# Kernel optimization log

Hardware: AMD Instinct MI355X
Metric: run time of the kernel (lower is better)

Reference implementation:

```python
import jax, jax.numpy as jnp
import numpy as np

N_SYN = 30_000_000
N_POST = 200_000
N_SOURCE = 17_400


def setup_inputs() -> dict:
    key = jax.random.key(0)
    k1, k2, k3, k4 = jax.random.split(key, 4)
    # spike input: ~half of source neurons active (values in {0,1})
    inputs_t = jax.random.randint(k1, (1, N_SOURCE), 0, 2, dtype=jnp.int32)
    # synapse table: col0 = postsynaptic neuron id, col1 = presynaptic source id
    post = jax.random.randint(k2, (N_SYN, 1), 0, N_POST, dtype=jnp.int32)
    pre = jax.random.randint(k3, (N_SYN, 1), 0, N_SOURCE, dtype=jnp.int32)
    indices = jnp.concatenate([post, pre], axis=1)  # [N_SYN, 2]
    weights = jax.random.normal(k4, (N_SYN,), dtype=jnp.float32)
    return {"inputs_t": inputs_t, "indices": indices, "weights": weights, "n_post": N_POST}


def reference(inputs_t, indices, weights, n_post):
    # Original TF code: find active presynaptic columns (inputs_t > 0), gather all
    # synapses whose presynaptic neuron is active (ragged lookup + argsort), then
    # unsorted_segment_sum their weights by postsynaptic id. Mathematically this is:
    #   i_in[post] = sum_{syn : inputs_t[pre[syn]] > 0} weights[syn]
    # which we express as a masked gather + segment_sum (same math, jit-safe).
    active = (inputs_t[0] > 0)                      # [n_source] bool
    pre = indices[:, 1]                             # [n_syn]
    post = indices[:, 0]                            # [n_syn]
    contrib = weights * active[pre].astype(weights.dtype)  # [n_syn]
    i_in = jax.ops.segment_sum(contrib, post, num_segments=n_post)  # [n_post]
    return i_in[None, :]                            # [1, n_post]
```

## Files before the change

kernel.cpp:

```cpp
#include <hip/hip_runtime.h>


typedef int   vint4   __attribute__((ext_vector_type(4)));
typedef float vfloat4 __attribute__((ext_vector_type(4)));
typedef unsigned int uint;

#define P1_BLK    256
#define P1_ITER   12
#define CHUNK     (P1_BLK * P1_ITER * 4)
#define MINICAP   30
#define NB_MAX    392
#define STRIDE_MAX 11744
#define NW_MAX    544
#define P2_BLK    1024
#define NBLK_MAX  2448

__global__ __launch_bounds__(256) void p0_bitmask(
    const int* __restrict__ act, uint* __restrict__ bits_g, int n_src)
{
    int w  = blockIdx.x * blockDim.x + threadIdx.x;
    int nw = (n_src + 31) >> 5;
    if (w < nw) {
        uint m = 0;
        int base = w << 5;
        #pragma unroll
        for (int j = 0; j < 32; ++j) {
            int s = base + j;
            if (s < n_src && act[s] > 0) m |= (1u << j);
        }
        bits_g[w] = m;
    }
}

__global__ __launch_bounds__(P1_BLK) void p1_bucketize(
    const uint* __restrict__ bits_g,
    const vint4* __restrict__ idx4,
    const vfloat4* __restrict__ w4,
    uint* __restrict__ cnt_g,
    uint* __restrict__ pairs_g,
    float* __restrict__ out,
    int sec_base_vec, int sec_nvec, int blocks_s, int nb, int nwords, int stride_dw)
{
    __shared__ uint bits[NW_MAX];
    __shared__ uint cnt[NB_MAX];
    __shared__ __align__(16) uint ord[STRIDE_MAX];

    const int tid = threadIdx.x;
    for (int i = tid; i < nwords; i += P1_BLK) bits[i] = bits_g[i];
    for (int i = tid; i < nb;     i += P1_BLK) cnt[i] = 0;
    __syncthreads();

    const int vbase = sec_base_vec + blockIdx.x * (P1_ITER * P1_BLK);

    for (int it = 0; it < P1_ITER; ++it) {
        int v = vbase + it * P1_BLK + tid;
        if ((v - sec_base_vec) < sec_nvec) {
            vint4   ia = __builtin_nontemporal_load(&idx4[2 * v]);
            vint4   ib = __builtin_nontemporal_load(&idx4[2 * v + 1]);
            vfloat4 wv = __builtin_nontemporal_load(&w4[v]);

            const int   posts[4] = {ia.x, ia.z, ib.x, ib.z};
            const int   pres[4]  = {ia.y, ia.w, ib.y, ib.w};
            const float wsv[4]   = {wv.x, wv.y, wv.z, wv.w};

            #pragma unroll
            for (int j = 0; j < 4; ++j) {
                uint pre = (uint)pres[j];
                if ((bits[pre >> 5] >> (pre & 31u)) & 1u) {
                    uint post = (uint)posts[j];
                    uint b    = post >> 9;
                    uint r    = atomicAdd(&cnt[b], 1u);
                    if (r < MINICAP) {
                        uint pk = (__float_as_uint(wsv[j]) & 0xFFFFFE00u) | (post & 511u);
                        ord[b * MINICAP + r] = pk;
                    } else {
                        atomicAdd(&out[post], wsv[j]);
                    }
                }
            }
        }
    }
    __syncthreads();

    for (int b = tid; b < nb; b += P1_BLK) {
        uint c = cnt[b];
        cnt_g[(size_t)b * (size_t)blocks_s + blockIdx.x] = (c > MINICAP) ? MINICAP : c;
    }
    vint4* dst = (vint4*)(pairs_g + (size_t)blockIdx.x * (size_t)stride_dw);
    const vint4* src = (const vint4*)ord;
    for (int i = tid; i < (stride_dw >> 2); i += P1_BLK)
        dst[i] = src[i];
}

__global__ __launch_bounds__(P2_BLK) void p2_accum(
    const uint* __restrict__ pairs_g,
    const uint* __restrict__ cnt_g,
    float* __restrict__ out,
    int blocks_s, int nb, int stride_dw, int n_post)
{
    __shared__ float hist[512];
    __shared__ unsigned short cntl[NBLK_MAX];

    const int b   = blockIdx.x;
    const int tid = threadIdx.x;
    for (int i = tid; i < 512; i += P2_BLK) hist[i] = 0.f;
    for (int i = tid; i < blocks_s; i += P2_BLK)
        cntl[i] = (unsigned short)cnt_g[(size_t)b * (size_t)blocks_s + i];
    __syncthreads();

    const int total = blocks_s * MINICAP;
    const size_t bucket_off = (size_t)b * MINICAP;
    for (int i = tid; i < total; i += P2_BLK) {
        int blk  = i / MINICAP;
        int slot = i - blk * MINICAP;
        if (slot < (int)cntl[blk]) {
            uint pk = pairs_g[(size_t)blk * (size_t)stride_dw + bucket_off + slot];
            atomicAdd(&hist[pk & 511u], __uint_as_float(pk & 0xFFFFFE00u));
        }
    }
    __syncthreads();

    for (int l = tid; l < 512; l += P2_BLK) {
        int g = (b << 9) + l;
        if (g < n_post) out[g] += hist[l];
    }
}

__global__ __launch_bounds__(256) void syn_scatter_direct(
    const int* __restrict__ act, const vint4* __restrict__ idx4,
    const vfloat4* __restrict__ w4, float* __restrict__ out, int n_vec)
{
    int t = blockIdx.x * blockDim.x + threadIdx.x;
    if (t >= n_vec) return;
    vint4 ia = idx4[2 * t], ib = idx4[2 * t + 1];
    vfloat4 wv = w4[t];
    if (act[ia.y] > 0) atomicAdd(&out[ia.x], wv.x);
    if (act[ia.w] > 0) atomicAdd(&out[ia.z], wv.y);
    if (act[ib.y] > 0) atomicAdd(&out[ib.x], wv.z);
    if (act[ib.w] > 0) atomicAdd(&out[ib.z], wv.w);
}

extern "C" void kernel_launch(void* const* d_in, const int* in_sizes, int n_in,
                              void* d_out, int out_size, void* d_ws, size_t ws_size,
                              hipStream_t stream) {
    const int*   act     = (const int*)d_in[0];
    const int*   indices = (const int*)d_in[1];
    const float* weights = (const float*)d_in[2];

    const int n_src  = in_sizes[0];
    const int n_syn  = in_sizes[2];
    const int n_post = out_size;
    const int n_vec  = n_syn / 4;

    const int nb        = (n_post + 511) >> 9;
    const int nwords    = (n_src + 31) >> 5;
    const int stride_dw = (nb * MINICAP + 31) & ~31;
    const int nblk_tot  = (n_syn + CHUNK - 1) / CHUNK;

    const size_t per_blk_bytes = (size_t)nb * 4 + (size_t)stride_dw * 4;
    const size_t head_bytes    = 4096;
    long long nblk_fit = (ws_size > head_bytes)
                       ? (long long)((ws_size - head_bytes) / per_blk_bytes) : 0;

    bool ok = (n_syn % 4 == 0) && (nb <= NB_MAX - 1) && (nwords <= NW_MAX) &&
              (stride_dw <= STRIDE_MAX) && (nblk_tot <= NBLK_MAX) && (nblk_fit >= 1);
    int nsec = ok ? (int)((nblk_tot + nblk_fit - 1) / nblk_fit) : 1000;

    if (!ok || nsec > 8) {
        (void)hipMemsetAsync(d_out, 0, (size_t)n_post * sizeof(float), stream);
        const int grid = (n_vec + 255) / 256;
        syn_scatter_direct<<<grid, 256, 0, stream>>>(
            act, (const vint4*)indices, (const vfloat4*)weights, (float*)d_out, n_vec);
        return;
    }

    const int nblk_s = (nblk_tot + nsec - 1) / nsec;
    uint* bits_g = (uint*)d_ws;
    uint* cnt_g  = (uint*)((char*)d_ws + head_bytes);
    size_t cnt_bytes = ((size_t)nb * (size_t)nblk_s * 4 + 255) & ~(size_t)255;
    uint* pairs_g = (uint*)((char*)cnt_g + cnt_bytes);

    (void)hipMemsetAsync(d_out, 0, (size_t)n_post * sizeof(float), stream);
    p0_bitmask<<<(nwords + 255) / 256, 256, 0, stream>>>(act, bits_g, n_src);

    const int vec_per_sec = nblk_s * (CHUNK / 4);
    for (int s = 0; s < nsec; ++s) {
        int v0 = s * vec_per_sec;
        int nv = n_vec - v0; if (nv > vec_per_sec) nv = vec_per_sec;
        if (nv <= 0) break;
        int blocks_s = (nv * 4 + CHUNK - 1) / CHUNK;
        p1_bucketize<<<blocks_s, P1_BLK, 0, stream>>>(
            bits_g, (const vint4*)indices, (const vfloat4*)weights,
            cnt_g, pairs_g, (float*)d_out,
            v0, nv, blocks_s, nb, nwords, stride_dw);
        p2_accum<<<nb, P2_BLK, 0, stream>>>(
            pairs_g, cnt_g, (float*)d_out, blocks_s, nb, stride_dw, n_post);
    }
}
```

Baseline: 517.0 us.

## Split bucket accumulation across blocks, pack counters, and software-pipeline bucketize loads

The bucket accumulation pass is split into SPLIT partial histograms per bucket, written to workspace and summed by a new merge kernel, so many more blocks work in parallel than one per bucket. The bucketize kernel shrinks its per-bucket capacity to 16 slots, packs two 16-bit counters per shared word to cut LDS use, sets an occupancy hint, and prefetches the next iteration's loads for full blocks. The accumulation pass now reads the packed pairs as 16-byte vectors. In exchange there are extra kernel launches, partial-sum traffic, and more overflow atomics to global memory because each bucket holds fewer slots.

```diff
diff --git a/kernel.cpp b/kernel.cpp
--- a/kernel.cpp
+++ b/kernel.cpp
@@ -6,14 +6,17 @@
 typedef unsigned int uint;
 
 #define P1_BLK    256
-#define P1_ITER   12
+#define P1_ITER   8
 #define CHUNK     (P1_BLK * P1_ITER * 4)
-#define MINICAP   30
+#define MINICAP   16
 #define NB_MAX    392
-#define STRIDE_MAX 11744
+#define CNTW      ((NB_MAX + 1) / 2)
+#define STRIDE_MAX 6272
 #define NW_MAX    544
-#define P2_BLK    1024
-#define NBLK_MAX  2448
+#define P2_BLK    512
+#define SPLIT     8
+#define NBLK_MAX  3664
+#define CBMAX     ((NBLK_MAX + SPLIT - 1) / SPLIT)
 
 __global__ __launch_bounds__(256) void p0_bitmask(
     const int* __restrict__ act, uint* __restrict__ bits_g, int n_src)
@@ -32,7 +35,7 @@
     }
 }
 
-__global__ __launch_bounds__(P1_BLK) void p1_bucketize(
+__global__ __launch_bounds__(P1_BLK, 5) void p1_bucketize(
     const uint* __restrict__ bits_g,
     const vint4* __restrict__ idx4,
     const vfloat4* __restrict__ w4,
@@ -42,48 +45,68 @@
     int sec_base_vec, int sec_nvec, int blocks_s, int nb, int nwords, int stride_dw)
 {
     __shared__ uint bits[NW_MAX];
-    __shared__ uint cnt[NB_MAX];
+    __shared__ uint cntp[CNTW];
     __shared__ __align__(16) uint ord[STRIDE_MAX];
 
     const int tid = threadIdx.x;
     for (int i = tid; i < nwords; i += P1_BLK) bits[i] = bits_g[i];
-    for (int i = tid; i < nb;     i += P1_BLK) cnt[i] = 0;
+    for (int i = tid; i < CNTW;   i += P1_BLK) cntp[i] = 0;
     __syncthreads();
 
     const int vbase = sec_base_vec + blockIdx.x * (P1_ITER * P1_BLK);
-
-    for (int it = 0; it < P1_ITER; ++it) {
-        int v = vbase + it * P1_BLK + tid;
-        if ((v - sec_base_vec) < sec_nvec) {
-            vint4   ia = __builtin_nontemporal_load(&idx4[2 * v]);
-            vint4   ib = __builtin_nontemporal_load(&idx4[2 * v + 1]);
-            vfloat4 wv = __builtin_nontemporal_load(&w4[v]);
-
-            const int   posts[4] = {ia.x, ia.z, ib.x, ib.z};
-            const int   pres[4]  = {ia.y, ia.w, ib.y, ib.w};
-            const float wsv[4]   = {wv.x, wv.y, wv.z, wv.w};
-
-            #pragma unroll
-            for (int j = 0; j < 4; ++j) {
-                uint pre = (uint)pres[j];
-                if ((bits[pre >> 5] >> (pre & 31u)) & 1u) {
-                    uint post = (uint)posts[j];
-                    uint b    = post >> 9;
-                    uint r    = atomicAdd(&cnt[b], 1u);
-                    if (r < MINICAP) {
-                        uint pk = (__float_as_uint(wsv[j]) & 0xFFFFFE00u) | (post & 511u);
-                        ord[b * MINICAP + r] = pk;
-                    } else {
-                        atomicAdd(&out[post], wsv[j]);
-                    }
+    const bool full = (vbase - sec_base_vec + P1_ITER * P1_BLK) <= sec_nvec;
+
+    auto process = [&](vint4 pa, vint4 pb, vfloat4 pw) {
+        const int   posts[4] = {pa.x, pa.z, pb.x, pb.z};
+        const int   pres[4]  = {pa.y, pa.w, pb.y, pb.w};
+        const float wsv[4]   = {pw.x, pw.y, pw.z, pw.w};
+        #pragma unroll
+        for (int j = 0; j < 4; ++j) {
+            uint pre = (uint)pres[j];
+            if ((bits[pre >> 5] >> (pre & 31u)) & 1u) {
+                uint post = (uint)posts[j];
+                uint b    = post >> 9;
+                uint sh   = (b & 1u) << 4;
+                uint r    = (atomicAdd(&cntp[b >> 1], 1u << sh) >> sh) & 0xFFFFu;
+                if (r < MINICAP) {
+                    uint pk = (__float_as_uint(wsv[j]) & 0xFFFFFE00u) | (post & 511u);
+                    ord[(b << 4) + r] = pk;
+                } else {
+                    atomicAdd(&out[post], wsv[j]);
                 }
             }
         }
+    };
+
+    if (full) {
+        int v = vbase + tid;
+        vint4   ia = __builtin_nontemporal_load(&idx4[2 * v]);
+        vint4   ib = __builtin_nontemporal_load(&idx4[2 * v + 1]);
+        vfloat4 wv = __builtin_nontemporal_load(&w4[v]);
+        for (int it = 0; it < P1_ITER - 1; ++it) {
+            int vn = v + P1_BLK;
+            vint4   na = __builtin_nontemporal_load(&idx4[2 * vn]);
+            vint4   nbv = __builtin_nontemporal_load(&idx4[2 * vn + 1]);
+            vfloat4 nw = __builtin_nontemporal_load(&w4[vn]);
+            process(ia, ib, wv);
+            ia = na; ib = nbv; wv = nw; v = vn;
+        }
+        process(ia, ib, wv);
+    } else {
+        for (int it = 0; it < P1_ITER; ++it) {
+            int v = vbase + it * P1_BLK + tid;
+            if ((v - sec_base_vec) < sec_nvec) {
+                vint4   ia = __builtin_nontemporal_load(&idx4[2 * v]);
+                vint4   ib = __builtin_nontemporal_load(&idx4[2 * v + 1]);
+                vfloat4 wv = __builtin_nontemporal_load(&w4[v]);
+                process(ia, ib, wv);
+            }
+        }
     }
     __syncthreads();
 
     for (int b = tid; b < nb; b += P1_BLK) {
-        uint c = cnt[b];
+        uint c = (cntp[b >> 1] >> ((b & 1u) << 4)) & 0xFFFFu;
         cnt_g[(size_t)b * (size_t)blocks_s + blockIdx.x] = (c > MINICAP) ? MINICAP : c;
     }
     vint4* dst = (vint4*)(pairs_g + (size_t)blockIdx.x * (size_t)stride_dw);
@@ -95,34 +118,60 @@
 __global__ __launch_bounds__(P2_BLK) void p2_accum(
     const uint* __restrict__ pairs_g,
     const uint* __restrict__ cnt_g,
-    float* __restrict__ out,
-    int blocks_s, int nb, int stride_dw, int n_post)
+    float* __restrict__ part,
+    int blocks_s, int nb, int stride_dw)
 {
     __shared__ float hist[512];
-    __shared__ unsigned short cntl[NBLK_MAX];
+    __shared__ unsigned short cntl[CBMAX];
 
     const int b   = blockIdx.x;
+    const int s   = blockIdx.y;
     const int tid = threadIdx.x;
-    for (int i = tid; i < 512; i += P2_BLK) hist[i] = 0.f;
-    for (int i = tid; i < blocks_s; i += P2_BLK)
-        cntl[i] = (unsigned short)cnt_g[(size_t)b * (size_t)blocks_s + i];
-    __syncthreads();
-
-    const int total = blocks_s * MINICAP;
-    const size_t bucket_off = (size_t)b * MINICAP;
+
+    const int chunk = (blocks_s + SPLIT - 1) / SPLIT;
+    const int blk0  = s * chunk;
+    int blkn = blocks_s - blk0;
+    if (blkn > chunk) blkn = chunk;
+    if (blkn < 0) blkn = 0;
+
+    for (int i = tid; i < 512;  i += P2_BLK) hist[i] = 0.f;
+    for (int i = tid; i < blkn; i += P2_BLK)
+        cntl[i] = (unsigned short)cnt_g[(size_t)b * (size_t)blocks_s + blk0 + i];
+    __syncthreads();
+
+    const int total = blkn << 2;
+    const uint boff = ((uint)b) << 4;
     for (int i = tid; i < total; i += P2_BLK) {
-        int blk  = i / MINICAP;
-        int slot = i - blk * MINICAP;
-        if (slot < (int)cntl[blk]) {
-            uint pk = pairs_g[(size_t)blk * (size_t)stride_dw + bucket_off + slot];
-            atomicAdd(&hist[pk & 511u], __uint_as_float(pk & 0xFFFFFE00u));
-        }
-    }
-    __syncthreads();
-
-    for (int l = tid; l < 512; l += P2_BLK) {
-        int g = (b << 9) + l;
-        if (g < n_post) out[g] += hist[l];
+        int bl = i >> 2;
+        int q  = i & 3;
+        const vint4* pv = (const vint4*)(pairs_g
+            + (size_t)(blk0 + bl) * (size_t)stride_dw + boff + (uint)(q << 2));
+        vint4 pk4 = *pv;
+        int c  = (int)cntl[bl];
+        int s0 = q << 2;
+        const uint pks[4] = {(uint)pk4.x, (uint)pk4.y, (uint)pk4.z, (uint)pk4.w};
+        #pragma unroll
+        for (int k = 0; k < 4; ++k) {
+            if (s0 + k < c)
+                atomicAdd(&hist[pks[k] & 511u], __uint_as_float(pks[k] & 0xFFFFFE00u));
+        }
+    }
+    __syncthreads();
+
+    float* dst = part + (size_t)s * ((size_t)nb << 9) + ((size_t)b << 9);
+    for (int l = tid; l < 512; l += P2_BLK) dst[l] = hist[l];
+}
+
+__global__ __launch_bounds__(256) void p3_merge(
+    const float* __restrict__ part, float* __restrict__ out, int n_post, int nb)
+{
+    int g = blockIdx.x * 256 + threadIdx.x;
+    if (g < n_post) {
+        size_t span = (size_t)nb << 9;
+        float acc = 0.f;
+        #pragma unroll
+        for (int k = 0; k < SPLIT; ++k) acc += part[(size_t)k * span + g];
+        out[g] += acc;
     }
 }
 
@@ -157,8 +206,9 @@
     const int stride_dw = (nb * MINICAP + 31) & ~31;
     const int nblk_tot  = (n_syn + CHUNK - 1) / CHUNK;
 
+    const size_t parts_bytes   = ((size_t)SPLIT * ((size_t)nb << 9) * 4 + 255) & ~(size_t)255;
+    const size_t head_bytes    = 4096 + parts_bytes;
     const size_t per_blk_bytes = (size_t)nb * 4 + (size_t)stride_dw * 4;
-    const size_t head_bytes    = 4096;
     long long nblk_fit = (ws_size > head_bytes)
                        ? (long long)((ws_size - head_bytes) / per_blk_bytes) : 0;
 
@@ -175,10 +225,11 @@
     }
 
     const int nblk_s = (nblk_tot + nsec - 1) / nsec;
-    uint* bits_g = (uint*)d_ws;
-    uint* cnt_g  = (uint*)((char*)d_ws + head_bytes);
+    uint*  bits_g = (uint*)d_ws;
+    float* parts  = (float*)((char*)d_ws + 4096);
+    uint*  cnt_g  = (uint*)((char*)d_ws + head_bytes);
     size_t cnt_bytes = ((size_t)nb * (size_t)nblk_s * 4 + 255) & ~(size_t)255;
-    uint* pairs_g = (uint*)((char*)cnt_g + cnt_bytes);
+    uint*  pairs_g = (uint*)((char*)cnt_g + cnt_bytes);
 
     (void)hipMemsetAsync(d_out, 0, (size_t)n_post * sizeof(float), stream);
     p0_bitmask<<<(nwords + 255) / 256, 256, 0, stream>>>(act, bits_g, n_src);
@@ -193,7 +244,9 @@
             bits_g, (const vint4*)indices, (const vfloat4*)weights,
             cnt_g, pairs_g, (float*)d_out,
             v0, nv, blocks_s, nb, nwords, stride_dw);
-        p2_accum<<<nb, P2_BLK, 0, stream>>>(
-            pairs_g, cnt_g, (float*)d_out, blocks_s, nb, stride_dw, n_post);
-    }
-}
+        p2_accum<<<dim3(nb, SPLIT), P2_BLK, 0, stream>>>(
+            pairs_g, cnt_g, parts, blocks_s, nb, stride_dw);
+        p3_merge<<<(n_post + 255) / 256, 256, 0, stream>>>(
+            parts, (float*)d_out, n_post, nb);
+    }
+}
```

Result: faster. 487.0 us (-5.8%).

## Replace bucketize/accumulate pipeline with per-XCC replicated output arrays

Applied to the files above, without the earlier changes.

Drops the two-phase LDS bucketing scheme (per-block bucket slots plus a second accumulation kernel). Instead, each block scatters atomics straight into one of 16 replicated output arrays, picked by the XCC id read from a hardware register and by block parity. A final merge kernel sums the replicas. This keeps atomic traffic local to each XCC's L2 and avoids contention and the pairs buffer round trip, at the cost of a 12.8MB memset and a merge pass.

```diff
diff --git a/kernel.cpp b/kernel.cpp
--- a/kernel.cpp
+++ b/kernel.cpp
@@ -5,15 +5,12 @@
 typedef float vfloat4 __attribute__((ext_vector_type(4)));
 typedef unsigned int uint;
 
-#define P1_BLK    256
-#define P1_ITER   12
-#define CHUNK     (P1_BLK * P1_ITER * 4)
-#define MINICAP   30
-#define NB_MAX    392
-#define STRIDE_MAX 11744
-#define NW_MAX    544
-#define P2_BLK    1024
-#define NBLK_MAX  2448
+#define NW_MAX 544
+#define REP    16
+#define P1_BLK 256
+#define P1_GRID_CAP 2048
+
+#define GETREG_XCC_ID (20 | (0 << 6) | (31 << 11))
 
 __global__ __launch_bounds__(256) void p0_bitmask(
     const int* __restrict__ act, uint* __restrict__ bits_g, int n_src)
@@ -32,97 +29,51 @@
     }
 }
 
-__global__ __launch_bounds__(P1_BLK) void p1_bucketize(
+__global__ __launch_bounds__(P1_BLK) void p1_scatter_rep(
     const uint* __restrict__ bits_g,
     const vint4* __restrict__ idx4,
     const vfloat4* __restrict__ w4,
-    uint* __restrict__ cnt_g,
-    uint* __restrict__ pairs_g,
-    float* __restrict__ out,
-    int sec_base_vec, int sec_nvec, int blocks_s, int nb, int nwords, int stride_dw)
+    float* __restrict__ rep,
+    int n_vec, int n_post, int nwords)
 {
     __shared__ uint bits[NW_MAX];
-    __shared__ uint cnt[NB_MAX];
-    __shared__ __align__(16) uint ord[STRIDE_MAX];
-
     const int tid = threadIdx.x;
     for (int i = tid; i < nwords; i += P1_BLK) bits[i] = bits_g[i];
-    for (int i = tid; i < nb;     i += P1_BLK) cnt[i] = 0;
     __syncthreads();
 
-    const int vbase = sec_base_vec + blockIdx.x * (P1_ITER * P1_BLK);
+    uint xcc = (uint)__builtin_amdgcn_s_getreg(GETREG_XCC_ID);
+    float* __restrict__ myrep =
+        rep + (size_t)(((xcc & 7u) << 1) | (blockIdx.x & 1u)) * (size_t)n_post;
 
-    for (int it = 0; it < P1_ITER; ++it) {
-        int v = vbase + it * P1_BLK + tid;
-        if ((v - sec_base_vec) < sec_nvec) {
-            vint4   ia = __builtin_nontemporal_load(&idx4[2 * v]);
-            vint4   ib = __builtin_nontemporal_load(&idx4[2 * v + 1]);
-            vfloat4 wv = __builtin_nontemporal_load(&w4[v]);
+    const int stride = gridDim.x * P1_BLK;
+    for (int v = blockIdx.x * P1_BLK + tid; v < n_vec; v += stride) {
+        vint4   ia = __builtin_nontemporal_load(&idx4[2 * v]);
+        vint4   ib = __builtin_nontemporal_load(&idx4[2 * v + 1]);
+        vfloat4 wv = __builtin_nontemporal_load(&w4[v]);
 
-            const int   posts[4] = {ia.x, ia.z, ib.x, ib.z};
-            const int   pres[4]  = {ia.y, ia.w, ib.y, ib.w};
-            const float wsv[4]   = {wv.x, wv.y, wv.z, wv.w};
+        const int   posts[4] = {ia.x, ia.z, ib.x, ib.z};
+        const int   pres[4]  = {ia.y, ia.w, ib.y, ib.w};
+        const float wsv[4]   = {wv.x, wv.y, wv.z, wv.w};
 
-            #pragma unroll
-            for (int j = 0; j < 4; ++j) {
-                uint pre = (uint)pres[j];
-                if ((bits[pre >> 5] >> (pre & 31u)) & 1u) {
-                    uint post = (uint)posts[j];
-                    uint b    = post >> 9;
-                    uint r    = atomicAdd(&cnt[b], 1u);
-                    if (r < MINICAP) {
-                        uint pk = (__float_as_uint(wsv[j]) & 0xFFFFFE00u) | (post & 511u);
-                        ord[b * MINICAP + r] = pk;
-                    } else {
-                        atomicAdd(&out[post], wsv[j]);
-                    }
-                }
-            }
+        #pragma unroll
+        for (int j = 0; j < 4; ++j) {
+            uint pre = (uint)pres[j];
+            if ((bits[pre >> 5] >> (pre & 31u)) & 1u)
+                atomicAdd(&myrep[(uint)posts[j]], wsv[j]);
         }
     }
-    __syncthreads();
-
-    for (int b = tid; b < nb; b += P1_BLK) {
-        uint c = cnt[b];
-        cnt_g[(size_t)b * (size_t)blocks_s + blockIdx.x] = (c > MINICAP) ? MINICAP : c;
-    }
-    vint4* dst = (vint4*)(pairs_g + (size_t)blockIdx.x * (size_t)stride_dw);
-    const vint4* src = (const vint4*)ord;
-    for (int i = tid; i < (stride_dw >> 2); i += P1_BLK)
-        dst[i] = src[i];
 }
 
-__global__ __launch_bounds__(P2_BLK) void p2_accum(
-    const uint* __restrict__ pairs_g,
-    const uint* __restrict__ cnt_g,
-    float* __restrict__ out,
-    int blocks_s, int nb, int stride_dw, int n_post)
+__global__ __launch_bounds__(256) void p3_merge_rep(
+    const float* __restrict__ rep, float* __restrict__ out, int n_post)
 {
-    __shared__ float hist[512];
-    __shared__ unsigned short cntl[NBLK_MAX];
-
-    const int b   = blockIdx.x;
-    const int tid = threadIdx.x;
-    for (int i = tid; i < 512; i += P2_BLK) hist[i] = 0.f;
-    for (int i = tid; i < blocks_s; i += P2_BLK)
-        cntl[i] = (unsigned short)cnt_g[(size_t)b * (size_t)blocks_s + i];
-    __syncthreads();
-
-    const int total = blocks_s * MINICAP;
-    const size_t bucket_off = (size_t)b * MINICAP;
-    for (int i = tid; i < total; i += P2_BLK) {
-        int blk  = i / MINICAP;
-        int slot = i - blk * MINICAP;
-        if (slot < (int)cntl[blk]) {
-            uint pk = pairs_g[(size_t)blk * (size_t)stride_dw + bucket_off + slot];
-            atomicAdd(&hist[pk & 511u], __uint_as_float(pk & 0xFFFFFE00u));
-        }
-    }
-    __syncthreads();
-
-    for (int l = tid; l < 512; l += P2_BLK) {
-        int g = (b << 9) + l;
-        if (g < n_post) out[g] += hist[l];
+    int g = blockIdx.x * 256 + threadIdx.x;
+    if (g < n_post) {
+        float acc = 0.f;
+        const float* p = rep + g;
+        #pragma unroll
+        for (int k = 0; k < REP; ++k) acc += p[(size_t)k * (size_t)n_post];
+        out[g] = acc;
     }
 }
 
@@ -152,21 +103,14 @@
     const int n_post = out_size;
     const int n_vec  = n_syn / 4;
 
-    const int nb        = (n_post + 511) >> 9;
-    const int nwords    = (n_src + 31) >> 5;
-    const int stride_dw = (nb * MINICAP + 31) & ~31;
-    const int nblk_tot  = (n_syn + CHUNK - 1) / CHUNK;
+    const int nwords = (n_src + 31) >> 5;
 
-    const size_t per_blk_bytes = (size_t)nb * 4 + (size_t)stride_dw * 4;
-    const size_t head_bytes    = 4096;
-    long long nblk_fit = (ws_size > head_bytes)
-                       ? (long long)((ws_size - head_bytes) / per_blk_bytes) : 0;
+    const size_t rep_bytes = (size_t)REP * (size_t)n_post * sizeof(float);
+    const size_t need      = 4096 + rep_bytes;
 
-    bool ok = (n_syn % 4 == 0) && (nb <= NB_MAX - 1) && (nwords <= NW_MAX) &&
-              (stride_dw <= STRIDE_MAX) && (nblk_tot <= NBLK_MAX) && (nblk_fit >= 1);
-    int nsec = ok ? (int)((nblk_tot + nblk_fit - 1) / nblk_fit) : 1000;
+    bool ok = (n_syn % 4 == 0) && (nwords <= NW_MAX) && (ws_size >= need);
 
-    if (!ok || nsec > 8) {
+    if (!ok) {
         (void)hipMemsetAsync(d_out, 0, (size_t)n_post * sizeof(float), stream);
         const int grid = (n_vec + 255) / 256;
         syn_scatter_direct<<<grid, 256, 0, stream>>>(
@@ -174,26 +118,18 @@
         return;
     }
 
-    const int nblk_s = (nblk_tot + nsec - 1) / nsec;
-    uint* bits_g = (uint*)d_ws;
-    uint* cnt_g  = (uint*)((char*)d_ws + head_bytes);
-    size_t cnt_bytes = ((size_t)nb * (size_t)nblk_s * 4 + 255) & ~(size_t)255;
-    uint* pairs_g = (uint*)((char*)cnt_g + cnt_bytes);
+    uint*  bits_g = (uint*)d_ws;
+    float* rep    = (float*)((char*)d_ws + 4096);
 
-    (void)hipMemsetAsync(d_out, 0, (size_t)n_post * sizeof(float), stream);
+    (void)hipMemsetAsync(rep, 0, rep_bytes, stream);
     p0_bitmask<<<(nwords + 255) / 256, 256, 0, stream>>>(act, bits_g, n_src);
 
-    const int vec_per_sec = nblk_s * (CHUNK / 4);
-    for (int s = 0; s < nsec; ++s) {
-        int v0 = s * vec_per_sec;
-        int nv = n_vec - v0; if (nv > vec_per_sec) nv = vec_per_sec;
-        if (nv <= 0) break;
-        int blocks_s = (nv * 4 + CHUNK - 1) / CHUNK;
-        p1_bucketize<<<blocks_s, P1_BLK, 0, stream>>>(
-            bits_g, (const vint4*)indices, (const vfloat4*)weights,
-            cnt_g, pairs_g, (float*)d_out,
-            v0, nv, blocks_s, nb, nwords, stride_dw);
-        p2_accum<<<nb, P2_BLK, 0, stream>>>(
-            pairs_g, cnt_g, (float*)d_out, blocks_s, nb, stride_dw, n_post);
-    }
+    int grid = (n_vec + P1_BLK - 1) / P1_BLK;
+    if (grid > P1_GRID_CAP) grid = P1_GRID_CAP;
+    p1_scatter_rep<<<grid, P1_BLK, 0, stream>>>(
+        bits_g, (const vint4*)indices, (const vfloat4*)weights,
+        rep, n_vec, n_post, nwords);
+
+    p3_merge_rep<<<(n_post + 255) / 256, 256, 0, stream>>>(
+        rep, (float*)d_out, n_post);
 }
```

Result: slower. 1.050 ms (+103.1%).
